# Optimization experiments

Measured on AMD Instinct MI355X. Metric: run time of the kernel, lower is better.

Reference implementation:

```python
import jax, jax.numpy as jnp
import numpy as np

B, P_LEN, Q_LEN, HID = 8, 2048, 1024, 1024


def setup_inputs() -> dict:
    key = jax.random.key(0)
    k1, k2, k3, k4 = jax.random.split(key, 4)
    k = jax.random.normal(k1, (B, P_LEN, HID), dtype=jnp.float32)
    q = jax.random.normal(k2, (B, Q_LEN, HID), dtype=jnp.float32)
    # q_mask: True = pad token. All-valid mask (no pads) to avoid NaN rows.
    q_mask = jnp.zeros((B, Q_LEN), dtype=bool)
    # Xavier-normal-initialized Linear weights, shape [out, in] as in torch.
    std = float(np.sqrt(2.0 / (HID + HID)))
    Wk = jax.random.normal(k3, (HID, HID), dtype=jnp.float32) * std
    Wq = jax.random.normal(k4, (HID, HID), dtype=jnp.float32) * std
    return {"k": k, "q": q, "q_mask": q_mask, "Wk": Wk, "Wq": Wq}


def reference(k, q, q_mask, Wk, Wq):
    # relu-projected keys/queries (Linear has no bias)
    p_key = jax.nn.relu(jnp.einsum('bpd,hd->bph', k, Wk))   # [B, p_len, hid]
    q_key = jax.nn.relu(jnp.einsum('bqd,hd->bqh', q, Wq))   # [B, q_len, hid]
    scores = jnp.einsum('bph,bqh->bpq', p_key, q_key)        # [B, p_len, q_len]
    scores = jnp.where(q_mask[:, None, :], -jnp.inf, scores)
    alphas = jax.nn.softmax(scores, axis=-1)                 # [B, p_len, q_len]
    ctx = jnp.einsum('bpq,bqd->bpd', alphas, q)              # [B, p_len, q_dim]
    return ctx, alphas
```

## Files before the change

kernel.cpp:

```cpp
#include <hip/hip_runtime.h>
#include <hip/hip_bf16.h>
#include <math.h>


typedef _Float16 v8h __attribute__((ext_vector_type(8)));
typedef _Float16 v4h __attribute__((ext_vector_type(4)));
typedef float v4f __attribute__((ext_vector_type(4)));

#define AS1C(p) ((const __attribute__((address_space(1))) void*)(p))
#define AS3(p)  ((__attribute__((address_space(3))) void*)(p))

__global__ __launch_bounds__(512) void gemm_nt_f16_256(
    const _Float16* __restrict__ A, const _Float16* __restrict__ B,
    float* __restrict__ Cf, _Float16* __restrict__ Ch,
    int N, int K, int Mtiles, int Ntiles,
    long long sA, long long sB, long long sC, int relu)
{
  extern __shared__ _Float16 lds[];

  const int nwg = gridDim.x;
  const int cpx = nwg >> 3;
  const int bid = (blockIdx.x & 7) * cpx + (blockIdx.x >> 3);
  const int mt  = bid % Mtiles;
  const int nt  = (bid / Mtiles) % Ntiles;
  const int bz  = bid / (Mtiles * Ntiles);

  A += (long long)bz * sA;
  B += (long long)bz * sB;

  const int m0 = mt * 256;
  const int n0 = nt * 256;
  const int t  = threadIdx.x;
  const int l  = t & 63;
  const int w  = t >> 6;
  const int wm = (w >> 2) * 128;
  const int wn = (w & 3) * 64;
  const int fr = l & 15;
  const int fq = l >> 4;
  const int r3 = fr & 7;
  const int sa0 = (fq ^ r3) * 8;
  const int sa1 = ((4 + fq) ^ r3) * 8;

  const int trow = t >> 3;
  const int tswz = ((t & 7) ^ (trow & 7)) * 8;

  const _Float16* Ast = A + (long long)(m0 + trow) * K + tswz;
  const _Float16* Bst = B + (long long)(n0 + trow) * K + tswz;

  v4f acc[8][4];
#pragma unroll
  for (int i = 0; i < 8; ++i)
#pragma unroll
    for (int j = 0; j < 4; ++j)
      acc[i][j] = (v4f){0.f, 0.f, 0.f, 0.f};

  const int NT = K >> 6;

#define STAGE(kt) do {                                                                   \
    _Float16* s_ = lds + (((kt) & 1) << 15);                                             \
    const long long ko_ = (long long)((kt) << 6);                                        \
    __builtin_amdgcn_global_load_lds(AS1C(Ast + ko_),                AS3(s_ +         t * 8), 16, 0, 0); \
    __builtin_amdgcn_global_load_lds(AS1C(Ast +  64LL * K + ko_),    AS3(s_ +  4096 + t * 8), 16, 0, 0); \
    __builtin_amdgcn_global_load_lds(AS1C(Ast + 128LL * K + ko_),    AS3(s_ +  8192 + t * 8), 16, 0, 0); \
    __builtin_amdgcn_global_load_lds(AS1C(Ast + 192LL * K + ko_),    AS3(s_ + 12288 + t * 8), 16, 0, 0); \
    __builtin_amdgcn_global_load_lds(AS1C(Bst + ko_),                AS3(s_ + 16384 + t * 8), 16, 0, 0); \
    __builtin_amdgcn_global_load_lds(AS1C(Bst +  64LL * K + ko_),    AS3(s_ + 20480 + t * 8), 16, 0, 0); \
    __builtin_amdgcn_global_load_lds(AS1C(Bst + 128LL * K + ko_),    AS3(s_ + 24576 + t * 8), 16, 0, 0); \
    __builtin_amdgcn_global_load_lds(AS1C(Bst + 192LL * K + ko_),    AS3(s_ + 28672 + t * 8), 16, 0, 0); \
  } while (0)

  STAGE(0);

  for (int kt = 0; kt < NT; ++kt) {
    if (kt + 1 < NT) {
      STAGE(kt + 1);
      asm volatile("s_waitcnt vmcnt(8)" ::: "memory");
    } else {
      asm volatile("s_waitcnt vmcnt(0)" ::: "memory");
    }
    __builtin_amdgcn_sched_barrier(0);
    __builtin_amdgcn_s_barrier();
    asm volatile("" ::: "memory");

    const _Float16* Ab = lds + ((kt & 1) << 15);
    const _Float16* Bb = Ab + 16384;

    v8h a0[4], a1[4], b0[4], b1[4];

#pragma unroll
    for (int i = 0; i < 4; ++i) {
      a0[i] = *(const v8h*)&Ab[(wm + i * 16 + fr) * 64 + sa0];
      a1[i] = *(const v8h*)&Ab[(wm + i * 16 + fr) * 64 + sa1];
    }
#pragma unroll
    for (int j = 0; j < 2; ++j) {
      b0[j] = *(const v8h*)&Bb[(wn + j * 16 + fr) * 64 + sa0];
      b1[j] = *(const v8h*)&Bb[(wn + j * 16 + fr) * 64 + sa1];
    }
    __builtin_amdgcn_s_setprio(1);
#pragma unroll
    for (int i = 0; i < 4; ++i)
#pragma unroll
      for (int j = 0; j < 2; ++j) {
        acc[i][j] = __builtin_amdgcn_mfma_f32_16x16x32_f16(a0[i], b0[j], acc[i][j], 0, 0, 0);
        acc[i][j] = __builtin_amdgcn_mfma_f32_16x16x32_f16(a1[i], b1[j], acc[i][j], 0, 0, 0);
      }
    __builtin_amdgcn_s_setprio(0);

#pragma unroll
    for (int j = 2; j < 4; ++j) {
      b0[j] = *(const v8h*)&Bb[(wn + j * 16 + fr) * 64 + sa0];
      b1[j] = *(const v8h*)&Bb[(wn + j * 16 + fr) * 64 + sa1];
    }
    __builtin_amdgcn_s_setprio(1);
#pragma unroll
    for (int i = 0; i < 4; ++i)
#pragma unroll
      for (int j = 2; j < 4; ++j) {
        acc[i][j] = __builtin_amdgcn_mfma_f32_16x16x32_f16(a0[i], b0[j], acc[i][j], 0, 0, 0);
        acc[i][j] = __builtin_amdgcn_mfma_f32_16x16x32_f16(a1[i], b1[j], acc[i][j], 0, 0, 0);
      }
    __builtin_amdgcn_s_setprio(0);

#pragma unroll
    for (int i = 0; i < 4; ++i) {
      a0[i] = *(const v8h*)&Ab[(wm + 64 + i * 16 + fr) * 64 + sa0];
      a1[i] = *(const v8h*)&Ab[(wm + 64 + i * 16 + fr) * 64 + sa1];
    }
    __builtin_amdgcn_s_setprio(1);
#pragma unroll
    for (int i = 0; i < 4; ++i)
#pragma unroll
      for (int j = 2; j < 4; ++j) {
        acc[4 + i][j] = __builtin_amdgcn_mfma_f32_16x16x32_f16(a0[i], b0[j], acc[4 + i][j], 0, 0, 0);
        acc[4 + i][j] = __builtin_amdgcn_mfma_f32_16x16x32_f16(a1[i], b1[j], acc[4 + i][j], 0, 0, 0);
      }
    __builtin_amdgcn_s_setprio(0);

    __builtin_amdgcn_s_setprio(1);
#pragma unroll
    for (int i = 0; i < 4; ++i)
#pragma unroll
      for (int j = 0; j < 2; ++j) {
        acc[4 + i][j] = __builtin_amdgcn_mfma_f32_16x16x32_f16(a0[i], b0[j], acc[4 + i][j], 0, 0, 0);
        acc[4 + i][j] = __builtin_amdgcn_mfma_f32_16x16x32_f16(a1[i], b1[j], acc[4 + i][j], 0, 0, 0);
      }
    __builtin_amdgcn_s_setprio(0);

    asm volatile("s_waitcnt lgkmcnt(0)" ::: "memory");
    __builtin_amdgcn_sched_barrier(0);
    __builtin_amdgcn_s_barrier();
  }
#undef STAGE

  float* Cfb = Cf ? Cf + (long long)bz * sC : nullptr;
  _Float16* Chb = Ch ? Ch + (long long)bz * sC : nullptr;
#pragma unroll
  for (int mh = 0; mh < 2; ++mh) {
#pragma unroll
    for (int i = 0; i < 4; ++i) {
#pragma unroll
      for (int j = 0; j < 4; ++j) {
#pragma unroll
        for (int r = 0; r < 4; ++r) {
          const int row = m0 + wm + mh * 64 + i * 16 + fq * 4 + r;
          const int col = n0 + wn + j * 16 + fr;
          float v = acc[mh * 4 + i][j][r];
          if (relu) v = fmaxf(v, 0.f);
          if (Cfb) Cfb[(long long)row * N + col] = v;
          if (Chb) Chb[(long long)row * N + col] = (_Float16)v;
        }
      }
    }
  }
}

__global__ __launch_bounds__(256) void convert_all_kernel(
    const float* __restrict__ s0, _Float16* __restrict__ d0, int b0,
    const float* __restrict__ s1, _Float16* __restrict__ d1, int b1,
    const float* __restrict__ s2, _Float16* __restrict__ d2, int b2,
    const float* __restrict__ s3, _Float16* __restrict__ d3)
{
  int blk = blockIdx.x;
  const float* src;
  _Float16* dst;
  if (blk < b0)           { src = s0; dst = d0; }
  else if (blk < b0 + b1) { src = s1; dst = d1; blk -= b0; }
  else if (blk < b0 + b1 + b2) { src = s2; dst = d2; blk -= b0 + b1; }
  else                    { src = s3; dst = d3; blk -= b0 + b1 + b2; }
  const long long i = ((long long)blk * 256 + threadIdx.x) * 4;
  const float4 v = *(const float4*)(src + i);
  v4h o = {(_Float16)v.x, (_Float16)v.y, (_Float16)v.z, (_Float16)v.w};
  *(v4h*)(dst + i) = o;
}

__global__ __launch_bounds__(256) void transpose_f16_kernel(
    const float* __restrict__ q, _Float16* __restrict__ qT, int Q, int H)
{
  __shared__ float tile[64][65];
  const float* qb = q + (long long)blockIdx.z * Q * H;
  _Float16* qTb = qT + (long long)blockIdx.z * H * Q;
  const int q0 = blockIdx.x * 64, h0 = blockIdx.y * 64;
  const int t = threadIdx.x;
  const int tr = t >> 4, tc = (t & 15) << 2;
#pragma unroll
  for (int i = 0; i < 4; ++i) {
    const float4 v = *(const float4*)(qb + (long long)(q0 + tr + i * 16) * H + h0 + tc);
    tile[tr + i * 16][tc + 0] = v.x;
    tile[tr + i * 16][tc + 1] = v.y;
    tile[tr + i * 16][tc + 2] = v.z;
    tile[tr + i * 16][tc + 3] = v.w;
  }
  __syncthreads();
#pragma unroll
  for (int i = 0; i < 4; ++i) {
    const int hl = tr + i * 16;
    const int ql = tc;
    v4h o = {(_Float16)tile[ql + 0][hl], (_Float16)tile[ql + 1][hl],
             (_Float16)tile[ql + 2][hl], (_Float16)tile[ql + 3][hl]};
    *(v4h*)(qTb + (long long)(h0 + hl) * Q + q0 + ql) = o;
  }
}

__global__ __launch_bounds__(256) void softmax_rows_kernel(
    float* __restrict__ S, _Float16* __restrict__ S16,
    const unsigned char* __restrict__ qmask, int Q, int P)
{
  const long long row = blockIdx.x;
  const int b = (int)(row / P);
  float* s = S + row * (long long)Q;
  const unsigned char* msk = qmask + (long long)b * Q;
  const int t = threadIdx.x;
  float4 v = *(const float4*)(s + (t << 2));
  float vals[4] = {v.x, v.y, v.z, v.w};
#pragma unroll
  for (int j = 0; j < 4; ++j)
    if (msk[(t << 2) + j]) vals[j] = -INFINITY;

  __shared__ float red[8];
  const int wid = t >> 6, lid = t & 63;

  float mx = fmaxf(fmaxf(vals[0], vals[1]), fmaxf(vals[2], vals[3]));
#pragma unroll
  for (int o = 32; o > 0; o >>= 1) mx = fmaxf(mx, __shfl_xor(mx, o, 64));
  if (lid == 0) red[wid] = mx;
  __syncthreads();
  mx = fmaxf(fmaxf(red[0], red[1]), fmaxf(red[2], red[3]));

  float e[4];
  float sum = 0.f;
#pragma unroll
  for (int j = 0; j < 4; ++j) { e[j] = __expf(vals[j] - mx); sum += e[j]; }
#pragma unroll
  for (int o = 32; o > 0; o >>= 1) sum += __shfl_xor(sum, o, 64);
  __syncthreads();
  if (lid == 0) red[4 + wid] = sum;
  __syncthreads();
  sum = red[4] + red[5] + red[6] + red[7];
  const float inv = 1.f / sum;

  float4 o;
  o.x = e[0] * inv; o.y = e[1] * inv; o.z = e[2] * inv; o.w = e[3] * inv;
  *(float4*)(s + (t << 2)) = o;
  v4h oh = {(_Float16)o.x, (_Float16)o.y, (_Float16)o.z, (_Float16)o.w};
  *(v4h*)(S16 + row * (long long)Q + (t << 2)) = oh;
}

extern "C" void kernel_launch(void* const* d_in, const int* in_sizes, int n_in,
                              void* d_out, int out_size, void* d_ws, size_t ws_size,
                              hipStream_t stream)
{
  const int B = 8, P = 2048, Q = 1024, H = 1024;
  const float* k  = (const float*)d_in[0];
  const float* q  = (const float*)d_in[1];
  const unsigned char* qmask = (const unsigned char*)d_in[2];
  const float* Wk = (const float*)d_in[3];
  const float* Wq = (const float*)d_in[4];

  float* ctx    = (float*)d_out;
  float* alphas = ctx + (size_t)B * P * H;

  _Float16* pkey16 = (_Float16*)d_out;

  char* wsb = (char*)d_ws;
  _Float16* qkey16   = (_Float16*)(wsb);
  _Float16* k16      = (_Float16*)(wsb + 16777216);
  _Float16* alphas16 = k16;
  _Float16* q16      = (_Float16*)(wsb + 16777216 + 33554432);
  _Float16* qT16     = q16;
  _Float16* Wk16     = (_Float16*)(wsb + 67108864);
  _Float16* Wq16     = (_Float16*)(wsb + 69206016);

  const long long nK = (long long)B * P * H;
  const long long nQ = (long long)B * Q * H;
  const long long nW = (long long)H * H;

  const int bK = (int)(nK / 1024), bQ = (int)(nQ / 1024), bW = (int)(nW / 1024);
  convert_all_kernel<<<bK + bQ + 2 * bW, 256, 0, stream>>>(
      k, k16, bK, q, q16, bQ, Wk, Wk16, bW, Wq, Wq16);

  const size_t LDSB = 131072;
  gemm_nt_f16_256<<<64 * 4, 512, LDSB, stream>>>(
      k16, Wk16, nullptr, pkey16, H, H, 64, 4, 0LL, 0LL, 0LL, 1);
  gemm_nt_f16_256<<<32 * 4, 512, LDSB, stream>>>(
      q16, Wq16, nullptr, qkey16, H, H, 32, 4, 0LL, 0LL, 0LL, 1);
  gemm_nt_f16_256<<<8 * 4 * B, 512, LDSB, stream>>>(
      pkey16, qkey16, alphas, nullptr, Q, H, 8, 4,
      (long long)P * H, (long long)Q * H, (long long)P * Q, 0);
  transpose_f16_kernel<<<dim3(Q / 64, H / 64, B), 256, 0, stream>>>(q, qT16, Q, H);
  softmax_rows_kernel<<<B * P, 256, 0, stream>>>(alphas, alphas16, qmask, Q, P);
  gemm_nt_f16_256<<<8 * 4 * B, 512, LDSB, stream>>>(
      alphas16, qT16, ctx, nullptr, H, Q, 8, 4,
      (long long)P * Q, (long long)H * Q, (long long)P * H, 0);
}
```

Before: 387.4 us.

## Shrink GEMM tiles to 128x128 and merge both projection GEMMs into one launch

Replaces the 256x256, 512-thread GEMM with a 128x128, 256-thread variant that uses half the LDS (64KB). This yields many more workgroups per launch, to fill the CUs better and allow several blocks per CU. The K and Q projections now run in one launch: tile rows past mtSplit switch to the Wq weight and the qkey output, relying on q16 sitting right after k16 in the workspace. The cost is lower per-tile data reuse and more global traffic per FLOP.

```diff
diff --git a/kernel.cpp b/kernel.cpp
--- a/kernel.cpp
+++ b/kernel.cpp
@@ -10,9 +10,10 @@
 #define AS1C(p) ((const __attribute__((address_space(1))) void*)(p))
 #define AS3(p)  ((__attribute__((address_space(3))) void*)(p))
 
-__global__ __launch_bounds__(512) void gemm_nt_f16_256(
+__global__ __launch_bounds__(256) void gemm_nt_f16_128(
     const _Float16* __restrict__ A, const _Float16* __restrict__ B,
     float* __restrict__ Cf, _Float16* __restrict__ Ch,
+    const _Float16* __restrict__ B2, _Float16* __restrict__ Ch2, int mtSplit,
     int N, int K, int Mtiles, int Ntiles,
     long long sA, long long sB, long long sC, int relu)
 {
@@ -26,30 +27,35 @@
   const int bz  = bid / (Mtiles * Ntiles);
 
   A += (long long)bz * sA;
-  B += (long long)bz * sB;
-
-  const int m0 = mt * 256;
-  const int n0 = nt * 256;
-  const int t  = threadIdx.x;
-  const int l  = t & 63;
-  const int w  = t >> 6;
-  const int wm = (w >> 2) * 128;
-  const int wn = (w & 3) * 64;
-  const int fr = l & 15;
-  const int fq = l >> 4;
-  const int r3 = fr & 7;
+
+  const _Float16* Bp = B;
+  _Float16* Chp = Ch;
+  int m0c = mt * 128;
+  if (mt >= mtSplit) { Bp = B2; Chp = Ch2; m0c = (mt - mtSplit) * 128; }
+  Bp += (long long)bz * sB;
+
+  const int m0g = mt * 128;
+  const int n0  = nt * 128;
+  const int t   = threadIdx.x;
+  const int l   = t & 63;
+  const int w   = t >> 6;
+  const int wm  = (w >> 1) * 64;
+  const int wn  = (w & 1) * 64;
+  const int fr  = l & 15;
+  const int fq  = l >> 4;
+  const int r3  = fr & 7;
   const int sa0 = (fq ^ r3) * 8;
   const int sa1 = ((4 + fq) ^ r3) * 8;
 
   const int trow = t >> 3;
   const int tswz = ((t & 7) ^ (trow & 7)) * 8;
 
-  const _Float16* Ast = A + (long long)(m0 + trow) * K + tswz;
-  const _Float16* Bst = B + (long long)(n0 + trow) * K + tswz;
-
-  v4f acc[8][4];
-#pragma unroll
-  for (int i = 0; i < 8; ++i)
+  const _Float16* Ast = A  + (long long)(m0g + trow) * K + tswz;
+  const _Float16* Bst = Bp + (long long)(n0  + trow) * K + tswz;
+
+  v4f acc[4][4];
+#pragma unroll
+  for (int i = 0; i < 4; ++i)
 #pragma unroll
     for (int j = 0; j < 4; ++j)
       acc[i][j] = (v4f){0.f, 0.f, 0.f, 0.f};
@@ -57,16 +63,16 @@
   const int NT = K >> 6;
 
 #define STAGE(kt) do {                                                                   \
-    _Float16* s_ = lds + (((kt) & 1) << 15);                                             \
+    _Float16* s_ = lds + (((kt) & 1) << 14);                                             \
     const long long ko_ = (long long)((kt) << 6);                                        \
-    __builtin_amdgcn_global_load_lds(AS1C(Ast + ko_),                AS3(s_ +         t * 8), 16, 0, 0); \
-    __builtin_amdgcn_global_load_lds(AS1C(Ast +  64LL * K + ko_),    AS3(s_ +  4096 + t * 8), 16, 0, 0); \
-    __builtin_amdgcn_global_load_lds(AS1C(Ast + 128LL * K + ko_),    AS3(s_ +  8192 + t * 8), 16, 0, 0); \
-    __builtin_amdgcn_global_load_lds(AS1C(Ast + 192LL * K + ko_),    AS3(s_ + 12288 + t * 8), 16, 0, 0); \
-    __builtin_amdgcn_global_load_lds(AS1C(Bst + ko_),                AS3(s_ + 16384 + t * 8), 16, 0, 0); \
-    __builtin_amdgcn_global_load_lds(AS1C(Bst +  64LL * K + ko_),    AS3(s_ + 20480 + t * 8), 16, 0, 0); \
-    __builtin_amdgcn_global_load_lds(AS1C(Bst + 128LL * K + ko_),    AS3(s_ + 24576 + t * 8), 16, 0, 0); \
-    __builtin_amdgcn_global_load_lds(AS1C(Bst + 192LL * K + ko_),    AS3(s_ + 28672 + t * 8), 16, 0, 0); \
+    __builtin_amdgcn_global_load_lds(AS1C(Ast + ko_),               AS3(s_ +        t * 8), 16, 0, 0); \
+    __builtin_amdgcn_global_load_lds(AS1C(Ast + 32LL * K + ko_),    AS3(s_ + 2048 + t * 8), 16, 0, 0); \
+    __builtin_amdgcn_global_load_lds(AS1C(Ast + 64LL * K + ko_),    AS3(s_ + 4096 + t * 8), 16, 0, 0); \
+    __builtin_amdgcn_global_load_lds(AS1C(Ast + 96LL * K + ko_),    AS3(s_ + 6144 + t * 8), 16, 0, 0); \
+    __builtin_amdgcn_global_load_lds(AS1C(Bst + ko_),               AS3(s_ + 8192 + t * 8), 16, 0, 0); \
+    __builtin_amdgcn_global_load_lds(AS1C(Bst + 32LL * K + ko_),    AS3(s_ + 10240 + t * 8), 16, 0, 0); \
+    __builtin_amdgcn_global_load_lds(AS1C(Bst + 64LL * K + ko_),    AS3(s_ + 12288 + t * 8), 16, 0, 0); \
+    __builtin_amdgcn_global_load_lds(AS1C(Bst + 96LL * K + ko_),    AS3(s_ + 14336 + t * 8), 16, 0, 0); \
   } while (0)
 
   STAGE(0);
@@ -82,8 +88,8 @@
     __builtin_amdgcn_s_barrier();
     asm volatile("" ::: "memory");
 
-    const _Float16* Ab = lds + ((kt & 1) << 15);
-    const _Float16* Bb = Ab + 16384;
+    const _Float16* Ab = lds + ((kt & 1) << 14);
+    const _Float16* Bb = Ab + 8192;
 
     v8h a0[4], a1[4], b0[4], b1[4];
 
@@ -122,31 +128,6 @@
       }
     __builtin_amdgcn_s_setprio(0);
 
-#pragma unroll
-    for (int i = 0; i < 4; ++i) {
-      a0[i] = *(const v8h*)&Ab[(wm + 64 + i * 16 + fr) * 64 + sa0];
-      a1[i] = *(const v8h*)&Ab[(wm + 64 + i * 16 + fr) * 64 + sa1];
-    }
-    __builtin_amdgcn_s_setprio(1);
-#pragma unroll
-    for (int i = 0; i < 4; ++i)
-#pragma unroll
-      for (int j = 2; j < 4; ++j) {
-        acc[4 + i][j] = __builtin_amdgcn_mfma_f32_16x16x32_f16(a0[i], b0[j], acc[4 + i][j], 0, 0, 0);
-        acc[4 + i][j] = __builtin_amdgcn_mfma_f32_16x16x32_f16(a1[i], b1[j], acc[4 + i][j], 0, 0, 0);
-      }
-    __builtin_amdgcn_s_setprio(0);
-
-    __builtin_amdgcn_s_setprio(1);
-#pragma unroll
-    for (int i = 0; i < 4; ++i)
-#pragma unroll
-      for (int j = 0; j < 2; ++j) {
-        acc[4 + i][j] = __builtin_amdgcn_mfma_f32_16x16x32_f16(a0[i], b0[j], acc[4 + i][j], 0, 0, 0);
-        acc[4 + i][j] = __builtin_amdgcn_mfma_f32_16x16x32_f16(a1[i], b1[j], acc[4 + i][j], 0, 0, 0);
-      }
-    __builtin_amdgcn_s_setprio(0);
-
     asm volatile("s_waitcnt lgkmcnt(0)" ::: "memory");
     __builtin_amdgcn_sched_barrier(0);
     __builtin_amdgcn_s_barrier();
@@ -154,22 +135,19 @@
 #undef STAGE
 
   float* Cfb = Cf ? Cf + (long long)bz * sC : nullptr;
-  _Float16* Chb = Ch ? Ch + (long long)bz * sC : nullptr;
-#pragma unroll
-  for (int mh = 0; mh < 2; ++mh) {
-#pragma unroll
-    for (int i = 0; i < 4; ++i) {
-#pragma unroll
-      for (int j = 0; j < 4; ++j) {
-#pragma unroll
-        for (int r = 0; r < 4; ++r) {
-          const int row = m0 + wm + mh * 64 + i * 16 + fq * 4 + r;
-          const int col = n0 + wn + j * 16 + fr;
-          float v = acc[mh * 4 + i][j][r];
-          if (relu) v = fmaxf(v, 0.f);
-          if (Cfb) Cfb[(long long)row * N + col] = v;
-          if (Chb) Chb[(long long)row * N + col] = (_Float16)v;
-        }
+  _Float16* Chb = Chp ? Chp + (long long)bz * sC : nullptr;
+#pragma unroll
+  for (int i = 0; i < 4; ++i) {
+#pragma unroll
+    for (int j = 0; j < 4; ++j) {
+#pragma unroll
+      for (int r = 0; r < 4; ++r) {
+        const int row = m0c + wm + i * 16 + fq * 4 + r;
+        const int col = n0 + wn + j * 16 + fr;
+        float v = acc[i][j][r];
+        if (relu) v = fmaxf(v, 0.f);
+        if (Cfb) Cfb[(long long)row * N + col] = v;
+        if (Chb) Chb[(long long)row * N + col] = (_Float16)v;
       }
     }
   }
@@ -299,17 +277,16 @@
   convert_all_kernel<<<bK + bQ + 2 * bW, 256, 0, stream>>>(
       k, k16, bK, q, q16, bQ, Wk, Wk16, bW, Wq, Wq16);
 
-  const size_t LDSB = 131072;
-  gemm_nt_f16_256<<<64 * 4, 512, LDSB, stream>>>(
-      k16, Wk16, nullptr, pkey16, H, H, 64, 4, 0LL, 0LL, 0LL, 1);
-  gemm_nt_f16_256<<<32 * 4, 512, LDSB, stream>>>(
-      q16, Wq16, nullptr, qkey16, H, H, 32, 4, 0LL, 0LL, 0LL, 1);
-  gemm_nt_f16_256<<<8 * 4 * B, 512, LDSB, stream>>>(
-      pkey16, qkey16, alphas, nullptr, Q, H, 8, 4,
-      (long long)P * H, (long long)Q * H, (long long)P * Q, 0);
+  const size_t LDSB = 65536;
+  gemm_nt_f16_128<<<192 * 8, 256, LDSB, stream>>>(
+      k16, Wk16, nullptr, pkey16, Wq16, qkey16, 128,
+      H, H, 192, 8, 0LL, 0LL, 0LL, 1);
+  gemm_nt_f16_128<<<16 * 8 * B, 256, LDSB, stream>>>(
+      pkey16, qkey16, alphas, nullptr, qkey16, nullptr, 1 << 28,
+      Q, H, 16, 8, (long long)P * H, (long long)Q * H, (long long)P * Q, 0);
   transpose_f16_kernel<<<dim3(Q / 64, H / 64, B), 256, 0, stream>>>(q, qT16, Q, H);
   softmax_rows_kernel<<<B * P, 256, 0, stream>>>(alphas, alphas16, qmask, Q, P);
-  gemm_nt_f16_256<<<8 * 4 * B, 512, LDSB, stream>>>(
-      alphas16, qT16, ctx, nullptr, H, Q, 8, 4,
-      (long long)P * Q, (long long)H * Q, (long long)P * H, 0);
-}
+  gemm_nt_f16_128<<<16 * 8 * B, 256, LDSB, stream>>>(
+      alphas16, qT16, ctx, nullptr, qT16, nullptr, 1 << 28,
+      H, Q, 16, 8, (long long)P * Q, (long long)H * Q, (long long)P * H, 0);
+}
```

After: 380.1 us. Within noise of the previous version (-1.9%).

## Fuse key projection, scores, softmax and context into one per-row-block kernel

Applied to the files above, without the earlier changes.

A new kernel handles 64 p-rows per block. It computes the ReLU key projection into LDS, then the scores against precomputed q keys, applies the mask and softmax in registers, writes alphas, and runs the alphas-times-q GEMM, all inside that block. This removes the pkey round trip, the fp32 score write and reread, and the separate softmax pass. The query projection GEMM is moved to a smaller 128x128 tile variant. The cost is that every block streams the whole Wk, qkey and qT matrices from global/L2 without LDS staging or prefetch. It also runs with only 256 blocks at one block per CU and a large LDS footprint, so it may end up latency-bound.

```diff
diff --git a/kernel.cpp b/kernel.cpp
--- a/kernel.cpp
+++ b/kernel.cpp
@@ -9,8 +9,253 @@
 
 #define AS1C(p) ((const __attribute__((address_space(1))) void*)(p))
 #define AS3(p)  ((__attribute__((address_space(3))) void*)(p))
-
-__global__ __launch_bounds__(512) void gemm_nt_f16_256(
+#define MFMA16 __builtin_amdgcn_mfma_f32_16x16x32_f16
+
+__global__ __launch_bounds__(512) void fused_attn(
+    const _Float16* __restrict__ k16,
+    const _Float16* __restrict__ Wk16,
+    const _Float16* __restrict__ qkey16,
+    const _Float16* __restrict__ qT16,
+    const unsigned char* __restrict__ qmask,
+    float* __restrict__ ctx,
+    float* __restrict__ alphas)
+{
+  extern __shared__ _Float16 lds[];
+  _Float16* Pk   = lds;
+  _Float16* Sbuf = lds + 65536;
+  float*    red1 = (float*)(lds + 73728);
+  float*    red2 = (float*)(lds + 74752);
+
+  const int bz   = blockIdx.x & 7;
+  const int pblk = blockIdx.x >> 3;
+  const int p0   = pblk * 64;
+
+  const int t  = threadIdx.x;
+  const int l  = t & 63;
+  const int w  = t >> 6;
+  const int fr = l & 15;
+  const int fq = l >> 4;
+  const int w128 = w * 128;
+  const int sa0 = (fq ^ (fr & 7)) * 8;
+  const int sa1 = ((4 + fq) ^ (fr & 7)) * 8;
+
+  const int trow = t >> 3;
+  const int tswz = ((t & 7) ^ (trow & 7)) * 8;
+
+  const _Float16* Kst = k16 + ((long long)(bz * 2048 + p0 + trow)) * 1024 + tswz;
+  const _Float16* qkb = qkey16 + (long long)bz * 1048576;
+  const _Float16* qTb = qT16   + (long long)bz * 1048576;
+  float* ctxb = ctx    + (long long)(bz * 2048 + p0) * 1024;
+  float* alpb = alphas + (long long)(bz * 2048 + p0) * 1024;
+  const unsigned char* mskb = qmask + bz * 1024;
+
+  {
+    v4f acc0[8][4];
+#pragma unroll
+    for (int i = 0; i < 8; ++i)
+#pragma unroll
+      for (int j = 0; j < 4; ++j)
+        acc0[i][j] = (v4f){0.f, 0.f, 0.f, 0.f};
+
+#define STAGE0(kt) __builtin_amdgcn_global_load_lds( \
+      AS1C(Kst + ((long long)(kt) << 6)), AS3(Sbuf + (((kt) & 1) << 12) + t * 8), 16, 0, 0)
+
+    STAGE0(0);
+    for (int kt = 0; kt < 16; ++kt) {
+      if (kt < 15) {
+        STAGE0(kt + 1);
+        asm volatile("s_waitcnt vmcnt(1)" ::: "memory");
+      } else {
+        asm volatile("s_waitcnt vmcnt(0)" ::: "memory");
+      }
+      __builtin_amdgcn_sched_barrier(0);
+      __builtin_amdgcn_s_barrier();
+      asm volatile("" ::: "memory");
+
+      const _Float16* Bs = Sbuf + ((kt & 1) << 12);
+      v8h b0[4], b1[4];
+#pragma unroll
+      for (int j = 0; j < 4; ++j) {
+        b0[j] = *(const v8h*)&Bs[(j * 16 + fr) * 64 + sa0];
+        b1[j] = *(const v8h*)&Bs[(j * 16 + fr) * 64 + sa1];
+      }
+#pragma unroll
+      for (int i = 0; i < 8; ++i) {
+        const v8h a0 = *(const v8h*)&Wk16[(long long)(w128 + i * 16 + fr) * 1024 + kt * 64 + fq * 8];
+        const v8h a1 = *(const v8h*)&Wk16[(long long)(w128 + i * 16 + fr) * 1024 + kt * 64 + 32 + fq * 8];
+#pragma unroll
+        for (int j = 0; j < 4; ++j) {
+          acc0[i][j] = MFMA16(a0, b0[j], acc0[i][j], 0, 0, 0);
+          acc0[i][j] = MFMA16(a1, b1[j], acc0[i][j], 0, 0, 0);
+        }
+      }
+      asm volatile("s_waitcnt lgkmcnt(0)" ::: "memory");
+      __builtin_amdgcn_sched_barrier(0);
+      __builtin_amdgcn_s_barrier();
+    }
+#undef STAGE0
+
+#pragma unroll
+    for (int i = 0; i < 8; ++i) {
+#pragma unroll
+      for (int j = 0; j < 4; ++j) {
+        v4f v = acc0[i][j];
+        v4h h4 = {(_Float16)fmaxf(v[0], 0.f), (_Float16)fmaxf(v[1], 0.f),
+                  (_Float16)fmaxf(v[2], 0.f), (_Float16)fmaxf(v[3], 0.f)};
+        const int p   = j * 16 + fr;
+        const int s16 = w * 16 + i * 2 + (fq >> 1);
+        const int phys = (s16 & ~7) | ((s16 & 7) ^ (p & 7));
+        *(v4h*)&Pk[p * 1024 + phys * 8 + (fq & 1) * 4] = h4;
+      }
+    }
+    __syncthreads();
+  }
+
+  float M4[4], IV[4];
+  {
+    v4f acc[8][4];
+#pragma unroll
+    for (int i = 0; i < 8; ++i)
+#pragma unroll
+      for (int j = 0; j < 4; ++j)
+        acc[i][j] = (v4f){0.f, 0.f, 0.f, 0.f};
+
+    for (int kt = 0; kt < 16; ++kt) {
+      v8h pb0[4], pb1[4];
+#pragma unroll
+      for (int j = 0; j < 4; ++j) {
+        pb0[j] = *(const v8h*)&Pk[(j * 16 + fr) * 1024 + kt * 64 + sa0];
+        pb1[j] = *(const v8h*)&Pk[(j * 16 + fr) * 1024 + kt * 64 + sa1];
+      }
+#pragma unroll
+      for (int i = 0; i < 8; ++i) {
+        const v8h a0 = *(const v8h*)&qkb[(long long)(w128 + i * 16 + fr) * 1024 + kt * 64 + fq * 8];
+        const v8h a1 = *(const v8h*)&qkb[(long long)(w128 + i * 16 + fr) * 1024 + kt * 64 + 32 + fq * 8];
+#pragma unroll
+        for (int j = 0; j < 4; ++j) {
+          acc[i][j] = MFMA16(a0, pb0[j], acc[i][j], 0, 0, 0);
+          acc[i][j] = MFMA16(a1, pb1[j], acc[i][j], 0, 0, 0);
+        }
+      }
+    }
+
+#pragma unroll
+    for (int i = 0; i < 8; ++i) {
+      const unsigned m4 = *(const unsigned*)&mskb[w128 + i * 16 + fq * 4];
+      if (m4) {
+#pragma unroll
+        for (int r = 0; r < 4; ++r)
+          if ((m4 >> (8 * r)) & 0xFF) {
+#pragma unroll
+            for (int j = 0; j < 4; ++j) acc[i][j][r] = -INFINITY;
+          }
+      }
+    }
+
+#pragma unroll
+    for (int j = 0; j < 4; ++j) {
+      float pm = -INFINITY;
+#pragma unroll
+      for (int i = 0; i < 8; ++i) {
+        pm = fmaxf(pm, fmaxf(fmaxf(acc[i][j][0], acc[i][j][1]),
+                             fmaxf(acc[i][j][2], acc[i][j][3])));
+      }
+      pm = fmaxf(pm, __shfl_xor(pm, 16, 64));
+      pm = fmaxf(pm, __shfl_xor(pm, 32, 64));
+      if (fq == 0) red1[(j * 16 + fr) * 8 + w] = pm;
+    }
+    __syncthreads();
+#pragma unroll
+    for (int j = 0; j < 4; ++j) {
+      const float* r = &red1[(j * 16 + fr) * 8];
+      M4[j] = fmaxf(fmaxf(fmaxf(r[0], r[1]), fmaxf(r[2], r[3])),
+                    fmaxf(fmaxf(r[4], r[5]), fmaxf(r[6], r[7])));
+    }
+
+#pragma unroll
+    for (int j = 0; j < 4; ++j) {
+      float ps = 0.f;
+#pragma unroll
+      for (int i = 0; i < 8; ++i) {
+#pragma unroll
+        for (int r = 0; r < 4; ++r) {
+          const float e = __expf(acc[i][j][r] - M4[j]);
+          acc[i][j][r] = e;
+          ps += e;
+        }
+      }
+      ps += __shfl_xor(ps, 16, 64);
+      ps += __shfl_xor(ps, 32, 64);
+      if (fq == 0) red2[(j * 16 + fr) * 8 + w] = ps;
+    }
+    __syncthreads();
+#pragma unroll
+    for (int j = 0; j < 4; ++j) {
+      const float* r = &red2[(j * 16 + fr) * 8];
+      IV[j] = 1.f / (r[0] + r[1] + r[2] + r[3] + r[4] + r[5] + r[6] + r[7]);
+    }
+
+#pragma unroll
+    for (int i = 0; i < 8; ++i) {
+#pragma unroll
+      for (int j = 0; j < 4; ++j) {
+        float4 o;
+        o.x = acc[i][j][0] * IV[j];
+        o.y = acc[i][j][1] * IV[j];
+        o.z = acc[i][j][2] * IV[j];
+        o.w = acc[i][j][3] * IV[j];
+        const int p = j * 16 + fr;
+        *(float4*)&alpb[(long long)p * 1024 + w128 + i * 16 + fq * 4] = o;
+        v4h h4 = {(_Float16)o.x, (_Float16)o.y, (_Float16)o.z, (_Float16)o.w};
+        const int s16  = w * 16 + i * 2 + (fq >> 1);
+        const int phys = (s16 & ~7) | ((s16 & 7) ^ (p & 7));
+        *(v4h*)&Pk[p * 1024 + phys * 8 + (fq & 1) * 4] = h4;
+      }
+    }
+    __syncthreads();
+  }
+
+  {
+    v4f acc2[4][8];
+#pragma unroll
+    for (int i = 0; i < 4; ++i)
+#pragma unroll
+      for (int j = 0; j < 8; ++j)
+        acc2[i][j] = (v4f){0.f, 0.f, 0.f, 0.f};
+
+    for (int kt = 0; kt < 16; ++kt) {
+      v8h pa0[4], pa1[4];
+#pragma unroll
+      for (int i = 0; i < 4; ++i) {
+        pa0[i] = *(const v8h*)&Pk[(i * 16 + fr) * 1024 + kt * 64 + sa0];
+        pa1[i] = *(const v8h*)&Pk[(i * 16 + fr) * 1024 + kt * 64 + sa1];
+      }
+#pragma unroll
+      for (int j = 0; j < 8; ++j) {
+        const v8h b0 = *(const v8h*)&qTb[(long long)(w128 + j * 16 + fr) * 1024 + kt * 64 + fq * 8];
+        const v8h b1 = *(const v8h*)&qTb[(long long)(w128 + j * 16 + fr) * 1024 + kt * 64 + 32 + fq * 8];
+#pragma unroll
+        for (int i = 0; i < 4; ++i) {
+          acc2[i][j] = MFMA16(pa0[i], b0, acc2[i][j], 0, 0, 0);
+          acc2[i][j] = MFMA16(pa1[i], b1, acc2[i][j], 0, 0, 0);
+        }
+      }
+    }
+
+#pragma unroll
+    for (int i = 0; i < 4; ++i) {
+#pragma unroll
+      for (int j = 0; j < 8; ++j) {
+#pragma unroll
+        for (int r = 0; r < 4; ++r) {
+          ctxb[(long long)(i * 16 + fq * 4 + r) * 1024 + w128 + j * 16 + fr] = acc2[i][j][r];
+        }
+      }
+    }
+  }
+}
+
+__global__ __launch_bounds__(256) void gemm_nt_f16_128(
     const _Float16* __restrict__ A, const _Float16* __restrict__ B,
     float* __restrict__ Cf, _Float16* __restrict__ Ch,
     int N, int K, int Mtiles, int Ntiles,
@@ -21,20 +266,20 @@
   const int nwg = gridDim.x;
   const int cpx = nwg >> 3;
   const int bid = (blockIdx.x & 7) * cpx + (blockIdx.x >> 3);
-  const int mt  = bid % Mtiles;
-  const int nt  = (bid / Mtiles) % Ntiles;
+  const int nt  = bid % Ntiles;
+  const int mt  = (bid / Ntiles) % Mtiles;
   const int bz  = bid / (Mtiles * Ntiles);
 
   A += (long long)bz * sA;
-  B += (long long)bz * sB;
-
-  const int m0 = mt * 256;
-  const int n0 = nt * 256;
+  const _Float16* Bp = B + (long long)bz * sB;
+
+  const int m0 = mt * 128;
+  const int n0 = nt * 128;
   const int t  = threadIdx.x;
   const int l  = t & 63;
   const int w  = t >> 6;
-  const int wm = (w >> 2) * 128;
-  const int wn = (w & 3) * 64;
+  const int wm = (w >> 1) * 64;
+  const int wn = (w & 1) * 64;
   const int fr = l & 15;
   const int fq = l >> 4;
   const int r3 = fr & 7;
@@ -44,12 +289,12 @@
   const int trow = t >> 3;
   const int tswz = ((t & 7) ^ (trow & 7)) * 8;
 
-  const _Float16* Ast = A + (long long)(m0 + trow) * K + tswz;
-  const _Float16* Bst = B + (long long)(n0 + trow) * K + tswz;
-
-  v4f acc[8][4];
-#pragma unroll
-  for (int i = 0; i < 8; ++i)
+  const _Float16* Ast = A  + (long long)(m0 + trow) * K + tswz;
+  const _Float16* Bst = Bp + (long long)(n0 + trow) * K + tswz;
+
+  v4f acc[4][4];
+#pragma unroll
+  for (int i = 0; i < 4; ++i)
 #pragma unroll
     for (int j = 0; j < 4; ++j)
       acc[i][j] = (v4f){0.f, 0.f, 0.f, 0.f};
@@ -57,16 +302,16 @@
   const int NT = K >> 6;
 
 #define STAGE(kt) do {                                                                   \
-    _Float16* s_ = lds + (((kt) & 1) << 15);                                             \
+    _Float16* s_ = lds + (((kt) & 1) << 14);                                             \
     const long long ko_ = (long long)((kt) << 6);                                        \
-    __builtin_amdgcn_global_load_lds(AS1C(Ast + ko_),                AS3(s_ +         t * 8), 16, 0, 0); \
-    __builtin_amdgcn_global_load_lds(AS1C(Ast +  64LL * K + ko_),    AS3(s_ +  4096 + t * 8), 16, 0, 0); \
-    __builtin_amdgcn_global_load_lds(AS1C(Ast + 128LL * K + ko_),    AS3(s_ +  8192 + t * 8), 16, 0, 0); \
-    __builtin_amdgcn_global_load_lds(AS1C(Ast + 192LL * K + ko_),    AS3(s_ + 12288 + t * 8), 16, 0, 0); \
-    __builtin_amdgcn_global_load_lds(AS1C(Bst + ko_),                AS3(s_ + 16384 + t * 8), 16, 0, 0); \
-    __builtin_amdgcn_global_load_lds(AS1C(Bst +  64LL * K + ko_),    AS3(s_ + 20480 + t * 8), 16, 0, 0); \
-    __builtin_amdgcn_global_load_lds(AS1C(Bst + 128LL * K + ko_),    AS3(s_ + 24576 + t * 8), 16, 0, 0); \
-    __builtin_amdgcn_global_load_lds(AS1C(Bst + 192LL * K + ko_),    AS3(s_ + 28672 + t * 8), 16, 0, 0); \
+    __builtin_amdgcn_global_load_lds(AS1C(Ast + ko_),            AS3(s_ +         t * 8), 16, 0, 0); \
+    __builtin_amdgcn_global_load_lds(AS1C(Ast + 32LL * K + ko_), AS3(s_ +  2048 + t * 8), 16, 0, 0); \
+    __builtin_amdgcn_global_load_lds(AS1C(Ast + 64LL * K + ko_), AS3(s_ +  4096 + t * 8), 16, 0, 0); \
+    __builtin_amdgcn_global_load_lds(AS1C(Ast + 96LL * K + ko_), AS3(s_ +  6144 + t * 8), 16, 0, 0); \
+    __builtin_amdgcn_global_load_lds(AS1C(Bst + ko_),            AS3(s_ +  8192 + t * 8), 16, 0, 0); \
+    __builtin_amdgcn_global_load_lds(AS1C(Bst + 32LL * K + ko_), AS3(s_ + 10240 + t * 8), 16, 0, 0); \
+    __builtin_amdgcn_global_load_lds(AS1C(Bst + 64LL * K + ko_), AS3(s_ + 12288 + t * 8), 16, 0, 0); \
+    __builtin_amdgcn_global_load_lds(AS1C(Bst + 96LL * K + ko_), AS3(s_ + 14336 + t * 8), 16, 0, 0); \
   } while (0)
 
   STAGE(0);
@@ -82,11 +327,10 @@
     __builtin_amdgcn_s_barrier();
     asm volatile("" ::: "memory");
 
-    const _Float16* Ab = lds + ((kt & 1) << 15);
-    const _Float16* Bb = Ab + 16384;
+    const _Float16* Ab = lds + ((kt & 1) << 14);
+    const _Float16* Bb = Ab + 8192;
 
     v8h a0[4], a1[4], b0[4], b1[4];
-
 #pragma unroll
     for (int i = 0; i < 4; ++i) {
       a0[i] = *(const v8h*)&Ab[(wm + i * 16 + fr) * 64 + sa0];
@@ -102,8 +346,8 @@
     for (int i = 0; i < 4; ++i)
 #pragma unroll
       for (int j = 0; j < 2; ++j) {
-        acc[i][j] = __builtin_amdgcn_mfma_f32_16x16x32_f16(a0[i], b0[j], acc[i][j], 0, 0, 0);
-        acc[i][j] = __builtin_amdgcn_mfma_f32_16x16x32_f16(a1[i], b1[j], acc[i][j], 0, 0, 0);
+        acc[i][j] = MFMA16(a0[i], b0[j], acc[i][j], 0, 0, 0);
+        acc[i][j] = MFMA16(a1[i], b1[j], acc[i][j], 0, 0, 0);
       }
     __builtin_amdgcn_s_setprio(0);
 
@@ -117,33 +361,8 @@
     for (int i = 0; i < 4; ++i)
 #pragma unroll
       for (int j = 2; j < 4; ++j) {
-        acc[i][j] = __builtin_amdgcn_mfma_f32_16x16x32_f16(a0[i], b0[j], acc[i][j], 0, 0, 0);
-        acc[i][j] = __builtin_amdgcn_mfma_f32_16x16x32_f16(a1[i], b1[j], acc[i][j], 0, 0, 0);
-      }
-    __builtin_amdgcn_s_setprio(0);
-
-#pragma unroll
-    for (int i = 0; i < 4; ++i) {
-      a0[i] = *(const v8h*)&Ab[(wm + 64 + i * 16 + fr) * 64 + sa0];
-      a1[i] = *(const v8h*)&Ab[(wm + 64 + i * 16 + fr) * 64 + sa1];
-    }
-    __builtin_amdgcn_s_setprio(1);
-#pragma unroll
-    for (int i = 0; i < 4; ++i)
-#pragma unroll
-      for (int j = 2; j < 4; ++j) {
-        acc[4 + i][j] = __builtin_amdgcn_mfma_f32_16x16x32_f16(a0[i], b0[j], acc[4 + i][j], 0, 0, 0);
-        acc[4 + i][j] = __builtin_amdgcn_mfma_f32_16x16x32_f16(a1[i], b1[j], acc[4 + i][j], 0, 0, 0);
-      }
-    __builtin_amdgcn_s_setprio(0);
-
-    __builtin_amdgcn_s_setprio(1);
-#pragma unroll
-    for (int i = 0; i < 4; ++i)
-#pragma unroll
-      for (int j = 0; j < 2; ++j) {
-        acc[4 + i][j] = __builtin_amdgcn_mfma_f32_16x16x32_f16(a0[i], b0[j], acc[4 + i][j], 0, 0, 0);
-        acc[4 + i][j] = __builtin_amdgcn_mfma_f32_16x16x32_f16(a1[i], b1[j], acc[4 + i][j], 0, 0, 0);
+        acc[i][j] = MFMA16(a0[i], b0[j], acc[i][j], 0, 0, 0);
+        acc[i][j] = MFMA16(a1[i], b1[j], acc[i][j], 0, 0, 0);
       }
     __builtin_amdgcn_s_setprio(0);
 
@@ -156,20 +375,17 @@
   float* Cfb = Cf ? Cf + (long long)bz * sC : nullptr;
   _Float16* Chb = Ch ? Ch + (long long)bz * sC : nullptr;
 #pragma unroll
-  for (int mh = 0; mh < 2; ++mh) {
-#pragma unroll
-    for (int i = 0; i < 4; ++i) {
-#pragma unroll
-      for (int j = 0; j < 4; ++j) {
-#pragma unroll
-        for (int r = 0; r < 4; ++r) {
-          const int row = m0 + wm + mh * 64 + i * 16 + fq * 4 + r;
-          const int col = n0 + wn + j * 16 + fr;
-          float v = acc[mh * 4 + i][j][r];
-          if (relu) v = fmaxf(v, 0.f);
-          if (Cfb) Cfb[(long long)row * N + col] = v;
-          if (Chb) Chb[(long long)row * N + col] = (_Float16)v;
-        }
+  for (int i = 0; i < 4; ++i) {
+#pragma unroll
+    for (int j = 0; j < 4; ++j) {
+#pragma unroll
+      for (int r = 0; r < 4; ++r) {
+        const int row = m0 + wm + i * 16 + fq * 4 + r;
+        const int col = n0 + wn + j * 16 + fr;
+        float v = acc[i][j][r];
+        if (relu) v = fmaxf(v, 0.f);
+        if (Cfb) Cfb[(long long)row * N + col] = v;
+        if (Chb) Chb[(long long)row * N + col] = (_Float16)v;
       }
     }
   }
@@ -222,50 +438,6 @@
   }
 }
 
-__global__ __launch_bounds__(256) void softmax_rows_kernel(
-    float* __restrict__ S, _Float16* __restrict__ S16,
-    const unsigned char* __restrict__ qmask, int Q, int P)
-{
-  const long long row = blockIdx.x;
-  const int b = (int)(row / P);
-  float* s = S + row * (long long)Q;
-  const unsigned char* msk = qmask + (long long)b * Q;
-  const int t = threadIdx.x;
-  float4 v = *(const float4*)(s + (t << 2));
-  float vals[4] = {v.x, v.y, v.z, v.w};
-#pragma unroll
-  for (int j = 0; j < 4; ++j)
-    if (msk[(t << 2) + j]) vals[j] = -INFINITY;
-
-  __shared__ float red[8];
-  const int wid = t >> 6, lid = t & 63;
-
-  float mx = fmaxf(fmaxf(vals[0], vals[1]), fmaxf(vals[2], vals[3]));
-#pragma unroll
-  for (int o = 32; o > 0; o >>= 1) mx = fmaxf(mx, __shfl_xor(mx, o, 64));
-  if (lid == 0) red[wid] = mx;
-  __syncthreads();
-  mx = fmaxf(fmaxf(red[0], red[1]), fmaxf(red[2], red[3]));
-
-  float e[4];
-  float sum = 0.f;
-#pragma unroll
-  for (int j = 0; j < 4; ++j) { e[j] = __expf(vals[j] - mx); sum += e[j]; }
-#pragma unroll
-  for (int o = 32; o > 0; o >>= 1) sum += __shfl_xor(sum, o, 64);
-  __syncthreads();
-  if (lid == 0) red[4 + wid] = sum;
-  __syncthreads();
-  sum = red[4] + red[5] + red[6] + red[7];
-  const float inv = 1.f / sum;
-
-  float4 o;
-  o.x = e[0] * inv; o.y = e[1] * inv; o.z = e[2] * inv; o.w = e[3] * inv;
-  *(float4*)(s + (t << 2)) = o;
-  v4h oh = {(_Float16)o.x, (_Float16)o.y, (_Float16)o.z, (_Float16)o.w};
-  *(v4h*)(S16 + row * (long long)Q + (t << 2)) = oh;
-}
-
 extern "C" void kernel_launch(void* const* d_in, const int* in_sizes, int n_in,
                               void* d_out, int out_size, void* d_ws, size_t ws_size,
                               hipStream_t stream)
@@ -280,16 +452,13 @@
   float* ctx    = (float*)d_out;
   float* alphas = ctx + (size_t)B * P * H;
 
-  _Float16* pkey16 = (_Float16*)d_out;
-
   char* wsb = (char*)d_ws;
-  _Float16* qkey16   = (_Float16*)(wsb);
-  _Float16* k16      = (_Float16*)(wsb + 16777216);
-  _Float16* alphas16 = k16;
-  _Float16* q16      = (_Float16*)(wsb + 16777216 + 33554432);
-  _Float16* qT16     = q16;
-  _Float16* Wk16     = (_Float16*)(wsb + 67108864);
-  _Float16* Wq16     = (_Float16*)(wsb + 69206016);
+  _Float16* qkey16 = (_Float16*)(wsb);
+  _Float16* k16    = (_Float16*)(wsb + 16777216);
+  _Float16* q16    = (_Float16*)(wsb + 16777216 + 33554432);
+  _Float16* qT16   = q16;
+  _Float16* Wk16   = (_Float16*)(wsb + 67108864);
+  _Float16* Wq16   = (_Float16*)(wsb + 69206016);
 
   const long long nK = (long long)B * P * H;
   const long long nQ = (long long)B * Q * H;
@@ -299,17 +468,11 @@
   convert_all_kernel<<<bK + bQ + 2 * bW, 256, 0, stream>>>(
       k, k16, bK, q, q16, bQ, Wk, Wk16, bW, Wq, Wq16);
 
-  const size_t LDSB = 131072;
-  gemm_nt_f16_256<<<64 * 4, 512, LDSB, stream>>>(
-      k16, Wk16, nullptr, pkey16, H, H, 64, 4, 0LL, 0LL, 0LL, 1);
-  gemm_nt_f16_256<<<32 * 4, 512, LDSB, stream>>>(
-      q16, Wq16, nullptr, qkey16, H, H, 32, 4, 0LL, 0LL, 0LL, 1);
-  gemm_nt_f16_256<<<8 * 4 * B, 512, LDSB, stream>>>(
-      pkey16, qkey16, alphas, nullptr, Q, H, 8, 4,
-      (long long)P * H, (long long)Q * H, (long long)P * Q, 0);
+  gemm_nt_f16_128<<<64 * 8, 256, 65536, stream>>>(
+      q16, Wq16, nullptr, qkey16, H, H, 64, 8, 0LL, 0LL, 0LL, 1);
+
   transpose_f16_kernel<<<dim3(Q / 64, H / 64, B), 256, 0, stream>>>(q, qT16, Q, H);
-  softmax_rows_kernel<<<B * P, 256, 0, stream>>>(alphas, alphas16, qmask, Q, P);
-  gemm_nt_f16_256<<<8 * 4 * B, 512, LDSB, stream>>>(
-      alphas16, qT16, ctx, nullptr, H, Q, 8, 4,
-      (long long)P * Q, (long long)H * Q, (long long)P * H, 0);
+
+  fused_attn<<<256, 512, 151552, stream>>>(
+      k16, Wk16, qkey16, qT16, qmask, ctx, alphas);
 }
```

Result: slower. 461.5 us (+19.1%).
